# Kernel tuning notes

Hardware: AMD Instinct MI355X
Metric: run time of the kernel (lower is better)

## Reference

```python
import jax, jax.numpy as jnp
import numpy as np

N_HEAD = 16


def setup_inputs() -> dict:
    key = jax.random.key(0)
    ks = jax.random.split(key, 5)
    B, T, C = 4, 2048, 1024
    s = 0.02
    return {
        "x": jax.random.normal(ks[0], (B, T, C), dtype=jnp.float32),
        "Wq": jax.random.normal(ks[1], (C, C), dtype=jnp.float32) * s,
        "Wk": jax.random.normal(ks[2], (C, C), dtype=jnp.float32) * s,
        "Wv": jax.random.normal(ks[3], (C, C), dtype=jnp.float32) * s,
        "Wp": jax.random.normal(ks[4], (C, C), dtype=jnp.float32) * s,
    }


def reference(x, Wq, Wk, Wv, Wp):
    B, T, C = x.shape
    H = N_HEAD
    D = C // H
    # torch Linear(bias=False): x @ W.T
    q = (x @ Wq.T).reshape(B, T, H, D).transpose(0, 2, 1, 3)  # [B,H,T,D]
    k = (x @ Wk.T).reshape(B, T, H, D).transpose(0, 2, 1, 3)
    v = (x @ Wv.T).reshape(B, T, H, D).transpose(0, 2, 1, 3)
    scale = 1.0 / jnp.sqrt(jnp.float32(D))
    att = jnp.einsum("bhqd,bhkd->bhqk", q, k) * scale  # [B,H,T,T]
    causal = jnp.tril(jnp.ones((T, T), dtype=bool))
    att = jnp.where(causal, att, jnp.float32(-jnp.inf))
    att = jax.nn.softmax(att, axis=-1)
    y = jnp.einsum("bhqk,bhkd->bhqd", att, v)  # [B,H,T,D]
    y = y.transpose(0, 2, 1, 3).reshape(B, T, C)
    return y @ Wp.T
```

## Files before the change

kernel.cpp:

```cpp
#include <hip/hip_runtime.h>
#include <hip/hip_bf16.h>
#include <math.h>

typedef __hip_bfloat16 bf16;
typedef __attribute__((ext_vector_type(8))) short short8;
typedef __attribute__((ext_vector_type(4))) float f32x4;
typedef __attribute__((ext_vector_type(2))) unsigned uint2v;
typedef __attribute__((ext_vector_type(4))) unsigned uint4v;

#define MFMA_BF16(a, b, c) __builtin_amdgcn_mfma_f32_16x16x32_bf16((a), (b), (c), 0, 0, 0)

__device__ __forceinline__ void async_copy16(const bf16* g, bf16* l) {
  __builtin_amdgcn_global_load_lds(
      (const __attribute__((address_space(1))) void*)g,
      (__attribute__((address_space(3))) void*)l,
      16, 0, 0);
}

__device__ __forceinline__ unsigned short f2bf_bits(float f) {
  bf16 h = __float2bfloat16(f);
  return *reinterpret_cast<unsigned short*>(&h);
}

__device__ __forceinline__ unsigned cvt_pk_bf16(float lo, float hi) {
  unsigned r;
  asm("v_cvt_pk_bf16_f32 %0, %1, %2" : "=v"(r) : "v"(lo), "v"(hi));
  return r;
}

__global__ __launch_bounds__(256) void cvt_all(const float* __restrict__ x,
                                               const float* __restrict__ wq,
                                               const float* __restrict__ wk,
                                               const float* __restrict__ wv,
                                               const float* __restrict__ wp,
                                               bf16* __restrict__ xb, bf16* __restrict__ wqb,
                                               bf16* __restrict__ wkb, bf16* __restrict__ wvb,
                                               bf16* __restrict__ wpb) {
  const int bid = blockIdx.x;
  const float* in;
  bf16* out;
  int off;
  float scale = 1.0f;
  if (bid < 8192) {
    in = x; out = xb; off = bid;
  } else if (bid < 9216) {
    in = wq; out = wqb; off = bid - 8192;
    scale = 0.180336880111112f;
  } else if (bid < 10240) {
    in = wk; out = wkb; off = bid - 9216;
  } else if (bid < 11264) {
    in = wv; out = wvb; off = bid - 10240;
  } else {
    in = wp; out = wpb; off = bid - 11264;
  }
  const int i = off * 256 + threadIdx.x;
  float4 v = reinterpret_cast<const float4*>(in)[i];
  ushort4 u;
  u.x = f2bf_bits(v.x * scale);
  u.y = f2bf_bits(v.y * scale);
  u.z = f2bf_bits(v.z * scale);
  u.w = f2bf_bits(v.w * scale);
  reinterpret_cast<ushort4*>(out)[i] = u;
}

template <int NZ>
__device__ __forceinline__ void gemm_fused_core(const bf16* __restrict__ A,
                                                const bf16* __restrict__ w0,
                                                const bf16* __restrict__ w1,
                                                const bf16* __restrict__ w2,
                                                int bx, int by,
                                                f32x4 (&acc)[NZ][4][4]) {
  __shared__ __align__(16) bf16 L[3][8192 + NZ * 4096];
  const int t = threadIdx.x;
  const int lane = t & 63;
  const int l15 = lane & 15;
  const int quad = (lane >> 4) & 3;
  const int wave = t >> 6;
  const int wm = (wave >> 1) * 64;
  const int wn = (wave & 1) * 64;
  const int K = 1024;

  const f32x4 zero = {0.f, 0.f, 0.f, 0.f};
#pragma unroll
  for (int z = 0; z < NZ; ++z)
#pragma unroll
    for (int m = 0; m < 4; ++m)
#pragma unroll
      for (int n = 0; n < 4; ++n) acc[z][m][n] = zero;

  const int srow = t >> 2;
  const int schunk = ((t & 3) ^ ((t >> 3) & 3)) * 8;
  const bf16* ga0 = A + (size_t)(by * 256 + srow) * K + schunk;
  const bf16* ga1 = ga0 + (size_t)128 * K;
  const bf16* ws[3] = {w0, w1, w2};
  const bf16* gw[NZ];
#pragma unroll
  for (int z = 0; z < NZ; ++z)
    gw[z] = ws[z] + (size_t)(bx * 128 + srow) * K + schunk;

  const int fsw = (quad ^ ((l15 >> 1) & 3)) * 8;
  const int arow = (wm + l15) * 32 + fsw;
  const int brow = (wn + l15) * 32 + fsw;

  auto stage = [&](int kt) {
    bf16* Ld = &L[kt % 3][0];
    async_copy16(ga0 + kt * 32, Ld + t * 8);
    async_copy16(ga1 + kt * 32, Ld + 4096 + t * 8);
#pragma unroll
    for (int z = 0; z < NZ; ++z)
      async_copy16(gw[z] + kt * 32, Ld + 8192 + z * 4096 + t * 8);
  };

  stage(0);
  stage(1);
  if constexpr (NZ == 3)
    asm volatile("s_waitcnt vmcnt(5)" ::: "memory");
  else
    asm volatile("s_waitcnt vmcnt(3)" ::: "memory");
  __builtin_amdgcn_s_barrier();

  for (int T = 0; T < 32; ++T) {
    const bf16* Lb = &L[T % 3][0];
    short8 af[4];
#pragma unroll
    for (int m = 0; m < 4; ++m)
      af[m] = *reinterpret_cast<const short8*>(Lb + arow + m * 512);
    if (T <= 29) {
      stage(T + 2);
      if constexpr (NZ == 3)
        asm volatile("s_waitcnt vmcnt(5)" ::: "memory");
      else
        asm volatile("s_waitcnt vmcnt(3)" ::: "memory");
    } else {
      asm volatile("s_waitcnt vmcnt(0)" ::: "memory");
    }
    __builtin_amdgcn_s_barrier();
    asm volatile("s_waitcnt lgkmcnt(0)" ::: "memory");
    __builtin_amdgcn_sched_barrier(0);
    __builtin_amdgcn_s_setprio(1);
#pragma unroll
    for (int z = 0; z < NZ; ++z) {
      short8 bfr[4];
#pragma unroll
      for (int n = 0; n < 4; ++n)
        bfr[n] = *reinterpret_cast<const short8*>(Lb + 8192 + z * 4096 + brow + n * 512);
#pragma unroll
      for (int m = 0; m < 4; ++m)
#pragma unroll
        for (int n = 0; n < 4; ++n) acc[z][m][n] = MFMA_BF16(af[m], bfr[n], acc[z][m][n]);
    }
    __builtin_amdgcn_s_setprio(0);
    __builtin_amdgcn_sched_barrier(0);
    __builtin_amdgcn_s_barrier();
  }
}

__device__ __forceinline__ void xcd_map(int i, int& bx, int& by) {
  bx = (i >> 3) & 7;
  by = (i & 7) * 4 + (i >> 6);
}

__global__ __launch_bounds__(512, 2) void gemm_qkv(const bf16* __restrict__ x,
                                                   const bf16* __restrict__ wq,
                                                   const bf16* __restrict__ wk,
                                                   const bf16* __restrict__ wv,
                                                   bf16* __restrict__ q, bf16* __restrict__ k,
                                                   bf16* __restrict__ vt) {
  int bx, by;
  xcd_map(blockIdx.x, bx, by);
  f32x4 acc[3][4][4];
  gemm_fused_core<3>(x, wq, wk, wv, bx, by, acc);
  const int t = threadIdx.x, lane = t & 63, l15 = lane & 15, quad = (lane >> 4) & 3,
            wave = t >> 6;
  const int wm = (wave >> 1) * 64, wn = (wave & 1) * 64;
  const int rb = by * 256 + wm + quad * 4;
  const int cbb = bx * 128 + wn + l15;
#pragma unroll
  for (int z = 0; z < 2; ++z) {
    bf16* C = z ? k : q;
#pragma unroll
    for (int m = 0; m < 4; ++m)
#pragma unroll
      for (int n = 0; n < 4; ++n)
#pragma unroll
        for (int r = 0; r < 4; ++r)
          C[(size_t)(rb + m * 16 + r) * 1024 + cbb + n * 16] = __float2bfloat16(acc[z][m][n][r]);
  }
#pragma unroll
  for (int m = 0; m < 4; ++m)
#pragma unroll
    for (int n = 0; n < 4; ++n) {
      const int tg = rb + m * 16;
      const int col = cbb + n * 16;
      const int b = tg >> 11, tl = tg & 2047;
      const int tls = (tl & ~12) | ((tl & 4) << 1) | ((tl & 8) >> 1);
      ushort4 pk;
      pk.x = f2bf_bits(acc[2][m][n][0]);
      pk.y = f2bf_bits(acc[2][m][n][1]);
      pk.z = f2bf_bits(acc[2][m][n][2]);
      pk.w = f2bf_bits(acc[2][m][n][3]);
      *reinterpret_cast<ushort4*>(&vt[((size_t)(b * 1024 + col)) * 2048 + tls]) = pk;
    }
}

__global__ __launch_bounds__(512, 2) void gemm_proj(const bf16* __restrict__ y,
                                                    const bf16* __restrict__ wp,
                                                    float* __restrict__ outp) {
  int bx, by;
  xcd_map(blockIdx.x, bx, by);
  f32x4 acc[1][4][4];
  gemm_fused_core<1>(y, wp, wp, wp, bx, by, acc);
  const int t = threadIdx.x, lane = t & 63, l15 = lane & 15, quad = (lane >> 4) & 3,
            wave = t >> 6;
  const int wm = (wave >> 1) * 64, wn = (wave & 1) * 64;
  const int rb = by * 256 + wm + quad * 4;
  const int cbb = bx * 128 + wn + l15;
#pragma unroll
  for (int m = 0; m < 4; ++m)
#pragma unroll
    for (int n = 0; n < 4; ++n)
#pragma unroll
      for (int r = 0; r < 4; ++r)
        outp[(size_t)(rb + m * 16 + r) * 1024 + cbb + n * 16] = acc[0][m][n][r];
}

__global__ __launch_bounds__(256) void attn(const bf16* __restrict__ qb,
                                            const bf16* __restrict__ kb,
                                            const bf16* __restrict__ vt,
                                            bf16* __restrict__ yb) {
  __shared__ __align__(16) bf16 Ks[2][2048];
  __shared__ __align__(16) bf16 Vs[2][2048];
  const int tid = threadIdx.x;
  const int lane = tid & 63, l15 = lane & 15, quad = lane >> 4, wave = tid >> 6;
  const int p = blockIdx.y;
  const int bh = blockIdx.x;
  const int b = bh >> 4, h = bh & 15;
  const size_t rowbase = (size_t)b * 2048;
  const int cb = h * 64;

  const int tlo = p, thi = 31 - p;
  const int gq0[2] = {tlo * 64 + wave * 16, thi * 64 + wave * 16};

  short8 aq[2][2];
#pragma unroll
  for (int g = 0; g < 2; ++g) {
    const bf16* qp = qb + (rowbase + gq0[g] + l15) * 1024 + cb + quad * 8;
    aq[g][0] = *reinterpret_cast<const short8*>(qp);
    aq[g][1] = *reinterpret_cast<const short8*>(qp + 32);
  }

  short8 ones;
#pragma unroll
  for (int i = 0; i < 8; ++i) ones[i] = (short)0x3F80;

  f32x4 o[2][4], l4[2];
  const f32x4 zero = {0.f, 0.f, 0.f, 0.f};
#pragma unroll
  for (int g = 0; g < 2; ++g) {
#pragma unroll
    for (int dt = 0; dt < 4; ++dt) o[g][dt] = zero;
    l4[g] = zero;
  }

  const int sdq = (((tid & 3) ^ ((tid >> 2) & 3) ^ ((tid >> 4) & 3))) * 8;
  const bf16* kg = kb + (rowbase + ((tid & 127) >> 2)) * 1024 + cb + (tid >> 7) * 32 + sdq;
  const bf16* vg = vt + ((size_t)bh * 64 + (tid >> 2)) * 2048 + sdq;
  const int csw = (quad ^ (l15 & 3) ^ ((l15 >> 2) & 3)) * 8;

  const int nkt = 2 * thi + 2;
  async_copy16(kg, &Ks[0][tid * 8]);
  async_copy16(vg, &Vs[0][tid * 8]);

  for (int kt = 0; kt < nkt; ++kt) {
    const int buf = kt & 1;
    __syncthreads();
    if (kt + 1 < nkt) {
      async_copy16(kg + (size_t)(kt + 1) * 32 * 1024, &Ks[buf ^ 1][tid * 8]);
      async_copy16(vg + (kt + 1) * 32, &Vs[buf ^ 1][tid * 8]);
    }
    const int k0g = kt * 32;
    if (k0g > gq0[1] + 15) continue;

    short8 bk[2][2];
#pragma unroll
    for (int j = 0; j < 2; ++j)
#pragma unroll
      for (int ks = 0; ks < 2; ++ks)
        bk[j][ks] = *reinterpret_cast<const short8*>(
            &Ks[buf][ks * 1024 + (j * 16 + l15) * 32 + csw]);
    short8 av[4];
#pragma unroll
    for (int dt = 0; dt < 4; ++dt)
      av[dt] = *reinterpret_cast<const short8*>(&Vs[buf][(dt * 16 + l15) * 32 + csw]);

#pragma unroll
    for (int g = 0; g < 2; ++g) {
      if (k0g > gq0[g] + 15) continue;
      f32x4 st[2];
#pragma unroll
      for (int j = 0; j < 2; ++j) {
        st[j] = MFMA_BF16(bk[j][0], aq[g][0], zero);
        st[j] = MFMA_BF16(bk[j][1], aq[g][1], st[j]);
      }
      const bool need_mask = (k0g + 31 > gq0[g]);
      unsigned w[2][2];
#pragma unroll
      for (int j = 0; j < 2; ++j) {
        float pw[4];
#pragma unroll
        for (int r = 0; r < 4; ++r) {
          float val = st[j][r];
          if (need_mask && (k0g + j * 16 + quad * 4 + r) > (gq0[g] + l15))
            val = -INFINITY;
          pw[r] = __builtin_amdgcn_exp2f(val);
        }
        w[j][0] = cvt_pk_bf16(pw[0], pw[1]);
        w[j][1] = cvt_pk_bf16(pw[2], pw[3]);
      }
      uint2v s0 = __builtin_amdgcn_permlane32_swap(w[0][0], w[1][0], false, false);
      uint2v s1 = __builtin_amdgcn_permlane32_swap(w[0][1], w[1][1], false, false);
      uint4v u;
      u[0] = s0[0];
      u[1] = s1[0];
      u[2] = s0[1];
      u[3] = s1[1];
      const short8 bp = __builtin_bit_cast(short8, u);
#pragma unroll
      for (int dt = 0; dt < 4; ++dt) o[g][dt] = MFMA_BF16(av[dt], bp, o[g][dt]);
      l4[g] = MFMA_BF16(ones, bp, l4[g]);
    }
  }

#pragma unroll
  for (int g = 0; g < 2; ++g) {
    const float invl = 1.f / l4[g][0];
    bf16* yp = yb + (rowbase + gq0[g] + l15) * 1024 + cb + quad * 4;
#pragma unroll
    for (int dt = 0; dt < 4; ++dt) {
      ushort4 pk;
      pk.x = f2bf_bits(o[g][dt][0] * invl);
      pk.y = f2bf_bits(o[g][dt][1] * invl);
      pk.z = f2bf_bits(o[g][dt][2] * invl);
      pk.w = f2bf_bits(o[g][dt][3] * invl);
      *reinterpret_cast<ushort4*>(&yp[dt * 16]) = pk;
    }
  }
}

extern "C" void kernel_launch(void* const* d_in, const int* in_sizes, int n_in,
                              void* d_out, int out_size, void* d_ws, size_t ws_size,
                              hipStream_t stream) {
  const float* x = (const float*)d_in[0];
  const float* Wq = (const float*)d_in[1];
  const float* Wk = (const float*)d_in[2];
  const float* Wv = (const float*)d_in[3];
  const float* Wp = (const float*)d_in[4];
  float* out = (float*)d_out;

  const size_t MB = 1024 * 1024;
  char* ws = (char*)d_ws;
  bf16* xb = (bf16*)(ws);
  bf16* qb = (bf16*)(ws + 16 * MB);
  bf16* kb = (bf16*)(ws + 32 * MB);
  bf16* vtb = (bf16*)(ws + 48 * MB);
  bf16* wqb = (bf16*)(ws + 64 * MB);
  bf16* wkb = (bf16*)(ws + 66 * MB);
  bf16* wvb = (bf16*)(ws + 68 * MB);
  bf16* wpb = (bf16*)(ws + 70 * MB);
  bf16* yb = xb;

  cvt_all<<<12288, 256, 0, stream>>>(x, Wq, Wk, Wv, Wp, xb, wqb, wkb, wvb, wpb);
  gemm_qkv<<<256, 512, 0, stream>>>(xb, wqb, wkb, wvb, qb, kb, vtb);
  attn<<<dim3(64, 16), 256, 0, stream>>>(qb, kb, vtb, yb);
  gemm_proj<<<256, 512, 0, stream>>>(yb, wpb, out);
}
```

Measured before the change: 258.7 us.

## Double attention KV tile to 64 keys with new XOR swizzle and occupancy hint

The attention kernel now stages 64 keys per iteration instead of 32, which halves the number of loop iterations and block barriers per query pair. The LDS layout is reorganised into 64-element rows with an XOR swizzle by row. V fragments are now loaded inside the PV loop rather than up front, and work on 16-key subtiles past the causal diagonal is skipped. A launch_bounds occupancy hint of 3 is added. In exchange, per-block LDS use doubles and register pressure rises, which could limit occupancy.

```diff
diff --git a/kernel.cpp b/kernel.cpp
--- a/kernel.cpp
+++ b/kernel.cpp
@@ -224,12 +224,12 @@
         outp[(size_t)(rb + m * 16 + r) * 1024 + cbb + n * 16] = acc[0][m][n][r];
 }
 
-__global__ __launch_bounds__(256) void attn(const bf16* __restrict__ qb,
-                                            const bf16* __restrict__ kb,
-                                            const bf16* __restrict__ vt,
-                                            bf16* __restrict__ yb) {
-  __shared__ __align__(16) bf16 Ks[2][2048];
-  __shared__ __align__(16) bf16 Vs[2][2048];
+__global__ __launch_bounds__(256, 3) void attn(const bf16* __restrict__ qb,
+                                               const bf16* __restrict__ kb,
+                                               const bf16* __restrict__ vt,
+                                               bf16* __restrict__ yb) {
+  __shared__ __align__(16) bf16 Ks[2][4096];
+  __shared__ __align__(16) bf16 Vs[2][4096];
   const int tid = threadIdx.x;
   const int lane = tid & 63, l15 = lane & 15, quad = lane >> 4, wave = tid >> 6;
   const int p = blockIdx.y;
@@ -262,72 +262,86 @@
     l4[g] = zero;
   }
 
-  const int sdq = (((tid & 3) ^ ((tid >> 2) & 3) ^ ((tid >> 4) & 3))) * 8;
-  const bf16* kg = kb + (rowbase + ((tid & 127) >> 2)) * 1024 + cb + (tid >> 7) * 32 + sdq;
-  const bf16* vg = vt + ((size_t)bh * 64 + (tid >> 2)) * 2048 + sdq;
-  const int csw = (quad ^ (l15 & 3) ^ ((l15 >> 2) & 3)) * 8;
-
-  const int nkt = 2 * thi + 2;
+  const int srow = tid >> 3;
+  const int sc = (tid & 7) ^ (srow & 7);
+  const bf16* kg = kb + (rowbase + srow) * 1024 + cb + sc * 8;
+  const bf16* vg = vt + ((size_t)bh * 64 + srow) * 2048 + sc * 8;
+  const int fx = l15 & 7;
+
+  const int nkt = thi + 1;
   async_copy16(kg, &Ks[0][tid * 8]);
+  async_copy16(kg + 32 * 1024, &Ks[0][2048 + tid * 8]);
   async_copy16(vg, &Vs[0][tid * 8]);
+  async_copy16(vg + (size_t)32 * 2048, &Vs[0][2048 + tid * 8]);
 
   for (int kt = 0; kt < nkt; ++kt) {
     const int buf = kt & 1;
     __syncthreads();
     if (kt + 1 < nkt) {
-      async_copy16(kg + (size_t)(kt + 1) * 32 * 1024, &Ks[buf ^ 1][tid * 8]);
-      async_copy16(vg + (kt + 1) * 32, &Vs[buf ^ 1][tid * 8]);
-    }
-    const int k0g = kt * 32;
-    if (k0g > gq0[1] + 15) continue;
-
-    short8 bk[2][2];
-#pragma unroll
-    for (int j = 0; j < 2; ++j)
+      const bf16* kgn = kg + (size_t)(kt + 1) * 64 * 1024;
+      const bf16* vgn = vg + (kt + 1) * 64;
+      async_copy16(kgn, &Ks[buf ^ 1][tid * 8]);
+      async_copy16(kgn + 32 * 1024, &Ks[buf ^ 1][2048 + tid * 8]);
+      async_copy16(vgn, &Vs[buf ^ 1][tid * 8]);
+      async_copy16(vgn + (size_t)32 * 2048, &Vs[buf ^ 1][2048 + tid * 8]);
+    }
+    const int k0g = kt * 64;
+
+    short8 bk[4][2];
+#pragma unroll
+    for (int j = 0; j < 4; ++j)
 #pragma unroll
       for (int ks = 0; ks < 2; ++ks)
         bk[j][ks] = *reinterpret_cast<const short8*>(
-            &Ks[buf][ks * 1024 + (j * 16 + l15) * 32 + csw]);
-    short8 av[4];
-#pragma unroll
-    for (int dt = 0; dt < 4; ++dt)
-      av[dt] = *reinterpret_cast<const short8*>(&Vs[buf][(dt * 16 + l15) * 32 + csw]);
+            &Ks[buf][(j * 16 + l15) * 64 + (((ks * 4 + quad) ^ fx)) * 8]);
 
 #pragma unroll
     for (int g = 0; g < 2; ++g) {
       if (k0g > gq0[g] + 15) continue;
-      f32x4 st[2];
-#pragma unroll
-      for (int j = 0; j < 2; ++j) {
+      f32x4 st[4];
+#pragma unroll
+      for (int j = 0; j < 4; ++j) {
         st[j] = MFMA_BF16(bk[j][0], aq[g][0], zero);
         st[j] = MFMA_BF16(bk[j][1], aq[g][1], st[j]);
       }
-      const bool need_mask = (k0g + 31 > gq0[g]);
-      unsigned w[2][2];
-#pragma unroll
-      for (int j = 0; j < 2; ++j) {
-        float pw[4];
-#pragma unroll
-        for (int r = 0; r < 4; ++r) {
-          float val = st[j][r];
-          if (need_mask && (k0g + j * 16 + quad * 4 + r) > (gq0[g] + l15))
-            val = -INFINITY;
-          pw[r] = __builtin_amdgcn_exp2f(val);
+      const int rem = gq0[g] + 15 - k0g;
+      const bool need_mask = (k0g + 63 > gq0[g]);
+      unsigned w[4][2] = {{0u, 0u}, {0u, 0u}, {0u, 0u}, {0u, 0u}};
+#pragma unroll
+      for (int j = 0; j < 4; ++j) {
+        if (j * 16 <= rem) {
+          float pw[4];
+#pragma unroll
+          for (int r = 0; r < 4; ++r) {
+            float val = st[j][r];
+            if (need_mask && (k0g + j * 16 + quad * 4 + r) > (gq0[g] + l15))
+              val = -INFINITY;
+            pw[r] = __builtin_amdgcn_exp2f(val);
+          }
+          w[j][0] = cvt_pk_bf16(pw[0], pw[1]);
+          w[j][1] = cvt_pk_bf16(pw[2], pw[3]);
         }
-        w[j][0] = cvt_pk_bf16(pw[0], pw[1]);
-        w[j][1] = cvt_pk_bf16(pw[2], pw[3]);
       }
-      uint2v s0 = __builtin_amdgcn_permlane32_swap(w[0][0], w[1][0], false, false);
-      uint2v s1 = __builtin_amdgcn_permlane32_swap(w[0][1], w[1][1], false, false);
-      uint4v u;
-      u[0] = s0[0];
-      u[1] = s1[0];
-      u[2] = s0[1];
-      u[3] = s1[1];
-      const short8 bp = __builtin_bit_cast(short8, u);
-#pragma unroll
-      for (int dt = 0; dt < 4; ++dt) o[g][dt] = MFMA_BF16(av[dt], bp, o[g][dt]);
-      l4[g] = MFMA_BF16(ones, bp, l4[g]);
+#pragma unroll
+      for (int half = 0; half < 2; ++half) {
+        uint2v s0 =
+            __builtin_amdgcn_permlane32_swap(w[2 * half][0], w[2 * half + 1][0], false, false);
+        uint2v s1 =
+            __builtin_amdgcn_permlane32_swap(w[2 * half][1], w[2 * half + 1][1], false, false);
+        uint4v u;
+        u[0] = s0[0];
+        u[1] = s1[0];
+        u[2] = s0[1];
+        u[3] = s1[1];
+        const short8 bp = __builtin_bit_cast(short8, u);
+#pragma unroll
+        for (int dt = 0; dt < 4; ++dt) {
+          const short8 av = *reinterpret_cast<const short8*>(
+              &Vs[buf][(dt * 16 + l15) * 64 + (((half * 4 + quad) ^ fx)) * 8]);
+          o[g][dt] = MFMA_BF16(av, bp, o[g][dt]);
+        }
+        l4[g] = MFMA_BF16(ones, bp, l4[g]);
+      }
     }
   }
 
```

After: 244.6 us. -5.4%, faster.
